# Kernel tuning notes

Hardware: AMD Instinct MI355X
Metric: run time of the kernel (lower is better)

## Reference

```python
import jax, jax.numpy as jnp
import numpy as np

N_ATOMS = 500_000
N_MOLS = 25_000
HID = 300
CONSTRAINT = 0.0  # per-molecule target total (e.g. neutral net charge)
W_SCALE = 0.05    # keep random-init activations tame


def setup_inputs() -> dict:
    key = jax.random.key(0)
    ks = jax.random.split(key, 6)
    hidden = jax.random.normal(ks[0], (N_ATOMS, HID), dtype=jnp.float32)
    seg_ids = jnp.sort(jax.random.randint(ks[1], (N_ATOMS,), 0, N_MOLS, dtype=jnp.int32))
    # output readout FFN: Linear(300->300) -> ReLU -> Linear(300->1)
    W1 = jax.random.normal(ks[2], (HID, HID), dtype=jnp.float32) * W_SCALE
    b1 = jnp.zeros((HID,), dtype=jnp.float32)
    W2 = jax.random.normal(ks[3], (HID, 1), dtype=jnp.float32) * W_SCALE
    b2 = jnp.zeros((1,), dtype=jnp.float32)
    # weights readout FFN (same architecture); bias=1 keeps segment weight sums positive
    V1 = jax.random.normal(ks[4], (HID, HID), dtype=jnp.float32) * W_SCALE
    vb1 = jnp.zeros((HID,), dtype=jnp.float32)
    V2 = jax.random.normal(ks[5], (HID, 1), dtype=jnp.float32) * W_SCALE
    vb2 = jnp.ones((1,), dtype=jnp.float32)
    return {"hidden": hidden, "seg_ids": seg_ids, "W1": W1, "b1": b1, "W2": W2,
            "b2": b2, "V1": V1, "vb1": vb1, "V2": V2, "vb2": vb2}


def _ffn(x, Wa, ba, Wb, bb):
    # dropout is identity in eval mode
    h = jax.nn.relu(x @ Wa + ba)
    return h @ Wb + bb  # [N, 1]


def reference(hidden, seg_ids, W1, b1, W2, b2, V1, vb1, V2, vb2):
    output = _ffn(hidden, W1, b1, W2, b2)    # [N, 1] raw per-atom predictions
    weights = _ffn(hidden, V1, vb1, V2, vb2) # [N, 1] per-atom correction weights
    # per-molecule segment sums (replaces the Python loop over a_scope)
    sum_o = jax.ops.segment_sum(output[:, 0], seg_ids, num_segments=N_MOLS)   # [M]
    sum_w = jax.ops.segment_sum(weights[:, 0], seg_ids, num_segments=N_MOLS)  # [M]
    sum_w = jnp.where(sum_w == 0, 1.0, sum_w)  # empty segments are skipped in the original
    corr = (CONSTRAINT - sum_o) / sum_w        # [M]
    out = output + weights * corr[seg_ids][:, None]  # [N, 1]
    return out
```

## Files before the change

### kernel.cpp

```cpp
#include <hip/hip_runtime.h>
#include <stdint.h>

#define N_ATOMS 500000
#define N_MOLS  25000
#define HID     300
#define BA      128
#define WS_ELE  102400

#define AROWB   616
#define A_BYTES (BA * AROWB)
#define B_OFF   A_BYTES
#define BUF_B   40960

typedef __attribute__((ext_vector_type(8)))  short          short8v;
typedef __attribute__((ext_vector_type(16))) float          f32x16;

static __device__ __forceinline__ unsigned short f2bf(float f) {
  unsigned int u = __float_as_uint(f);
  u += 0x7fffu + ((u >> 16) & 1u);
  return (unsigned short)(u >> 16);
}

static __device__ __forceinline__ void stage16(const char* gsrc, char* ldst, int ln) {
  __builtin_amdgcn_global_load_lds(
      (const __attribute__((address_space(1))) void*)(gsrc + ln * 16),
      (__attribute__((address_space(3))) void*)ldst, 16, 0, 0);
}

__global__ void prep_kernel(
    const float* __restrict__ W1, const float* __restrict__ V1,
    const float* __restrict__ b1, const float* __restrict__ vb1,
    const float* __restrict__ W2, const float* __restrict__ V2,
    unsigned short* __restrict__ W1s, unsigned short* __restrict__ V1s,
    float* __restrict__ b1p, float* __restrict__ vb1p,
    float* __restrict__ W2p, float* __restrict__ V2p,
    float* __restrict__ sums)
{
  const int t = blockIdx.x * 256 + threadIdx.x;
  if (t < 2 * WS_ELE) {
    const float* src = (t < WS_ELE) ? W1 : V1;
    unsigned short* dst = (t < WS_ELE) ? W1s : V1s;
    const int i    = (t < WS_ELE) ? t : t - WS_ELE;
    const int j    = i & 7;
    const int lane = (i >> 3) & 63;
    const int nt   = (i >> 9) % 10;
    const int kc16 = i / 5120;
    const int k = kc16 * 16 + (lane >> 5) * 8 + j;
    const int n = nt * 32 + (lane & 31);
    const float v = (k < HID && n < HID) ? src[k * HID + n] : 0.f;
    dst[i] = f2bf(v);
  } else if (t < 2 * WS_ELE + 1280) {
    const int i = t - 2 * WS_ELE;
    const int which = i / 320;
    const int e = i - which * 320;
    const float* s = (which == 0) ? b1 : (which == 1) ? vb1 : (which == 2) ? W2 : V2;
    float*       d = (which == 0) ? b1p : (which == 1) ? vb1p : (which == 2) ? W2p : V2p;
    d[e] = (e < HID) ? s[e] : 0.f;
  } else if (t < 2 * WS_ELE + 1280 + 2 * N_MOLS) {
    sums[t - (2 * WS_ELE + 1280)] = 0.f;
  }
}

__global__ __launch_bounds__(512, 2) void fused_ffn(
    const float* __restrict__ hidden,
    const unsigned short* __restrict__ W1s, const unsigned short* __restrict__ V1s,
    const float* __restrict__ b1p, const float* __restrict__ vb1p,
    const float* __restrict__ W2p, const float* __restrict__ V2p,
    const float* __restrict__ b2, const float* __restrict__ vb2,
    float* __restrict__ outA, float* __restrict__ outW)
{
  __shared__ char lds[A_BYTES + 2 * BUF_B];
  __shared__ float sOutA[BA];
  __shared__ float sOutW[BA];

  const int tid = (int)threadIdx.x;
  const int ln  = tid & 63;
  const int wv  = tid >> 6;
  const int mtx = wv & 1;
  const int ch  = (wv >> 1) & 1;
  const int rgh = wv >> 2;
  const int l31 = ln & 31;
  const int lh  = ln >> 5;
  const long base = (long)blockIdx.x * BA;

  {
    char* dst = lds + B_OFF;
    #pragma unroll
    for (int r = 0; r < 5; ++r) {
      const int cc = wv * 5 + r;
      const char* src = (cc < 20) ? ((const char*)W1s + cc * 1024)
                                  : ((const char*)V1s + (cc - 20) * 1024);
      stage16(src, dst + cc * 1024, ln);
    }
  }

  #pragma unroll
  for (int bt = 0; bt < 2; ++bt) {
    const int nb = bt ? 9 : 10;
    float4 tmp[10];
    #pragma unroll
    for (int m = 0; m < 10; ++m) {
      if (m >= nb) break;
      const int i   = tid + (bt * 10 + m) * 512;
      const int row = i / 76;
      const int c4  = i - row * 76;
      float4 v = make_float4(0.f, 0.f, 0.f, 0.f);
      const long atom = base + row;
      if (c4 < 75 && atom < N_ATOMS)
        v = *reinterpret_cast<const float4*>(hidden + atom * (long)HID + c4 * 4);
      tmp[m] = v;
    }
    #pragma unroll
    for (int m = 0; m < 10; ++m) {
      if (m >= nb) break;
      const int i   = tid + (bt * 10 + m) * 512;
      const int row = i / 76;
      const int c4  = i - row * 76;
      ushort4 b;
      b.x = f2bf(tmp[m].x); b.y = f2bf(tmp[m].y);
      b.z = f2bf(tmp[m].z); b.w = f2bf(tmp[m].w);
      *reinterpret_cast<ushort4*>(lds + row * AROWB + c4 * 8) = b;
    }
  }
  __syncthreads();

  f32x16 acc[2][5] = {};

  for (int c = 0; c < 10; ++c) {
    const char* buf = lds + B_OFF + (c & 1) * BUF_B;

    if (c < 9) {
      char* nbuf = lds + B_OFF + ((c + 1) & 1) * BUF_B;
      const char* wsrc = (const char*)W1s + (c + 1) * 20480;
      const char* vsrc = (const char*)V1s + (c + 1) * 20480;
      #pragma unroll
      for (int r = 0; r < 5; ++r) {
        const int cc = wv * 5 + r;
        const char* src = (cc < 20) ? (wsrc + cc * 1024) : (vsrc + (cc - 20) * 1024);
        stage16(src, nbuf + cc * 1024, ln);
      }
    }

#define DO_HALF(hh)                                                            \
    {                                                                          \
      const int kc16 = 2 * c + (hh);                                           \
      const short8v a0 = *reinterpret_cast<const short8v*>(                    \
          lds + (rgh * 64 + l31) * AROWB + kc16 * 32 + lh * 16);               \
      const short8v a1 = *reinterpret_cast<const short8v*>(                    \
          lds + (rgh * 64 + 32 + l31) * AROWB + kc16 * 32 + lh * 16);          \
      const char* bb = buf + mtx * 20480 + (hh) * 10240 + ch * 5120;           \
      _Pragma("unroll")                                                        \
      for (int nt = 0; nt < 5; ++nt) {                                         \
        const short8v bf = *reinterpret_cast<const short8v*>(                  \
            bb + nt * 1024 + ln * 16);                                         \
        acc[0][nt] = __builtin_amdgcn_mfma_f32_32x32x16_bf16(a0, bf, acc[0][nt], 0, 0, 0); \
        acc[1][nt] = __builtin_amdgcn_mfma_f32_32x32x16_bf16(a1, bf, acc[1][nt], 0, 0, 0); \
      }                                                                        \
    }
    DO_HALF(0);
    if (c < 9) DO_HALF(1);
#undef DO_HALF

    __syncthreads();
  }

  float bv[5], w2[5];
  const float* bbv = mtx ? vb1p : b1p;
  const float* ww2 = mtx ? V2p  : W2p;
  #pragma unroll
  for (int nt = 0; nt < 5; ++nt) {
    const int cix = ch * 160 + nt * 32 + l31;
    bv[nt] = bbv[cix];
    w2[nt] = ww2[cix];
  }
  if (tid < BA) { sOutA[tid] = 0.f; sOutW[tid] = 0.f; }
  __syncthreads();

  float* sOut = mtx ? sOutW : sOutA;
  #pragma unroll
  for (int rg = 0; rg < 2; ++rg) {
    #pragma unroll
    for (int r = 0; r < 16; ++r) {
      float s = 0.f;
      #pragma unroll
      for (int nt = 0; nt < 5; ++nt) {
        float x = fmaxf(acc[rg][nt][r] + bv[nt], 0.f);
        s = fmaf(x, w2[nt], s);
      }
      s += __shfl_xor(s, 1);
      s += __shfl_xor(s, 2);
      s += __shfl_xor(s, 4);
      s += __shfl_xor(s, 8);
      s += __shfl_xor(s, 16);
      if (l31 == 0) {
        const int row = rgh * 64 + rg * 32 + (r & 3) + 8 * (r >> 2) + 4 * lh;
        atomicAdd(&sOut[row], s);
      }
    }
  }
  __syncthreads();
  if (tid < BA) {
    const long atom = base + tid;
    if (atom < N_ATOMS) {
      outA[atom] = sOutA[tid] + b2[0];
      outW[atom] = sOutW[tid] + vb2[0];
    }
  }
}

__global__ void segsum_kernel(
    const float* __restrict__ outA, const float* __restrict__ outW,
    const int* __restrict__ seg,
    float* __restrict__ sum_o, float* __restrict__ sum_w)
{
  const long i0 = ((long)blockIdx.x * 256 + threadIdx.x) * 8;
  if (i0 >= N_ATOMS) return;
  const int4   s0 = *reinterpret_cast<const int4*>(seg + i0);
  const int4   s1 = *reinterpret_cast<const int4*>(seg + i0 + 4);
  const float4 o0 = *reinterpret_cast<const float4*>(outA + i0);
  const float4 o1 = *reinterpret_cast<const float4*>(outA + i0 + 4);
  const float4 w0 = *reinterpret_cast<const float4*>(outW + i0);
  const float4 w1 = *reinterpret_cast<const float4*>(outW + i0 + 4);
  const int   ss[8] = {s0.x, s0.y, s0.z, s0.w, s1.x, s1.y, s1.z, s1.w};
  const float oo[8] = {o0.x, o0.y, o0.z, o0.w, o1.x, o1.y, o1.z, o1.w};
  const float ww[8] = {w0.x, w0.y, w0.z, w0.w, w1.x, w1.y, w1.z, w1.w};
  int cur = ss[0];
  float ao = 0.f, aw = 0.f;
  #pragma unroll
  for (int j = 0; j < 8; ++j) {
    if (ss[j] != cur) {
      atomicAdd(&sum_o[cur], ao);
      atomicAdd(&sum_w[cur], aw);
      cur = ss[j]; ao = 0.f; aw = 0.f;
    }
    ao += oo[j]; aw += ww[j];
  }
  atomicAdd(&sum_o[cur], ao);
  atomicAdd(&sum_w[cur], aw);
}

__global__ void final_kernel(
    const float* __restrict__ outA, const float* __restrict__ outW,
    const int* __restrict__ seg,
    const float* __restrict__ sum_o, const float* __restrict__ sum_w,
    float* __restrict__ out)
{
  const long i0 = ((long)blockIdx.x * 256 + threadIdx.x) * 4;
  if (i0 >= N_ATOMS) return;
  const int4   s4 = *reinterpret_cast<const int4*>(seg + i0);
  const float4 o4 = *reinterpret_cast<const float4*>(outA + i0);
  const float4 w4 = *reinterpret_cast<const float4*>(outW + i0);
  const int   ss[4] = {s4.x, s4.y, s4.z, s4.w};
  const float oo[4] = {o4.x, o4.y, o4.z, o4.w};
  const float ww[4] = {w4.x, w4.y, w4.z, w4.w};
  float r[4];
  #pragma unroll
  for (int j = 0; j < 4; ++j) {
    const int s = ss[j];
    float sw = sum_w[s];
    sw = (sw == 0.f) ? 1.f : sw;
    const float corr = (0.f - sum_o[s]) / sw;
    r[j] = oo[j] + ww[j] * corr;
  }
  *reinterpret_cast<float4*>(out + i0) = make_float4(r[0], r[1], r[2], r[3]);
}

extern "C" void kernel_launch(void* const* d_in, const int* in_sizes, int n_in,
                              void* d_out, int out_size, void* d_ws, size_t ws_size,
                              hipStream_t stream)
{
  const float* hidden = (const float*)d_in[0];
  const int*   seg    = (const int*)d_in[1];
  const float* W1     = (const float*)d_in[2];
  const float* b1     = (const float*)d_in[3];
  const float* W2     = (const float*)d_in[4];
  const float* b2     = (const float*)d_in[5];
  const float* V1     = (const float*)d_in[6];
  const float* vb1    = (const float*)d_in[7];
  const float* V2     = (const float*)d_in[8];
  const float* vb2    = (const float*)d_in[9];

  char* ws = (char*)d_ws;
  float*          outA  = (float*)(ws + 0);
  float*          outW  = (float*)(ws + 2000000);
  float*          sum_o = (float*)(ws + 4000000);
  float*          sum_w = (float*)(ws + 4100000);
  unsigned short* W1s   = (unsigned short*)(ws + 4200000);
  unsigned short* V1s   = (unsigned short*)(ws + 4404800);
  float*          b1p   = (float*)(ws + 4609600);
  float*          vb1p  = (float*)(ws + 4610880);
  float*          W2p   = (float*)(ws + 4612160);
  float*          V2p   = (float*)(ws + 4613440);

  prep_kernel<<<1001, 256, 0, stream>>>(W1, V1, b1, vb1, W2, V2,
                                        W1s, V1s, b1p, vb1p, W2p, V2p, sum_o);

  const int nblk = (N_ATOMS + BA - 1) / BA;
  fused_ffn<<<nblk, 512, 0, stream>>>(hidden, W1s, V1s, b1p, vb1p, W2p, V2p,
                                      b2, vb2, outA, outW);

  segsum_kernel<<<(N_ATOMS / 8 + 255) / 256, 256, 0, stream>>>(outA, outW, seg,
                                                               sum_o, sum_w);

  final_kernel<<<(N_ATOMS / 4 + 255) / 256, 256, 0, stream>>>(outA, outW, seg,
                                                              sum_o, sum_w,
                                                              (float*)d_out);
}
```

Measured before the change: 418.6 us.

## Load weight fragments straight into registers and halve the atom tile

The fused FFN kernel no longer stages W1/V1 tiles through double-buffered LDS with global_load_lds and per-chunk barriers. Each wave now loads its B fragments directly from global (L2) into registers, prefetching the next k-chunk one step ahead. The block shrinks to 64 atoms and 256 threads, which cuts LDS use and removes the per-chunk __syncthreads. The cost is that weight traffic from L2 per atom doubles, and register pressure rises from holding the prefetched fragments. The input conversion also switches to the HIP bfloat16 intrinsic.

```diff
diff --git a/kernel.cpp b/kernel.cpp
--- a/kernel.cpp
+++ b/kernel.cpp
@@ -1,16 +1,14 @@
 #include <hip/hip_runtime.h>
+#include <hip/hip_bf16.h>
 #include <stdint.h>
 
 #define N_ATOMS 500000
 #define N_MOLS  25000
 #define HID     300
-#define BA      128
+#define BA      64
 #define WS_ELE  102400
-
+#define NCH     19
 #define AROWB   616
-#define A_BYTES (BA * AROWB)
-#define B_OFF   A_BYTES
-#define BUF_B   40960
 
 typedef __attribute__((ext_vector_type(8)))  short          short8v;
 typedef __attribute__((ext_vector_type(16))) float          f32x16;
@@ -19,12 +17,6 @@
   unsigned int u = __float_as_uint(f);
   u += 0x7fffu + ((u >> 16) & 1u);
   return (unsigned short)(u >> 16);
-}
-
-static __device__ __forceinline__ void stage16(const char* gsrc, char* ldst, int ln) {
-  __builtin_amdgcn_global_load_lds(
-      (const __attribute__((address_space(1))) void*)(gsrc + ln * 16),
-      (__attribute__((address_space(3))) void*)ldst, 16, 0, 0);
 }
 
 __global__ void prep_kernel(
@@ -61,7 +53,7 @@
   }
 }
 
-__global__ __launch_bounds__(512, 2) void fused_ffn(
+__global__ __launch_bounds__(256, 2) void fused_ffn(
     const float* __restrict__ hidden,
     const unsigned short* __restrict__ W1s, const unsigned short* __restrict__ V1s,
     const float* __restrict__ b1p, const float* __restrict__ vb1p,
@@ -69,7 +61,7 @@
     const float* __restrict__ b2, const float* __restrict__ vb2,
     float* __restrict__ outA, float* __restrict__ outW)
 {
-  __shared__ char lds[A_BYTES + 2 * BUF_B];
+  __shared__ char ldsA[BA * AROWB];
   __shared__ float sOutA[BA];
   __shared__ float sOutW[BA];
 
@@ -77,23 +69,11 @@
   const int ln  = tid & 63;
   const int wv  = tid >> 6;
   const int mtx = wv & 1;
-  const int ch  = (wv >> 1) & 1;
-  const int rgh = wv >> 2;
+  const int ch  = wv >> 1;
   const int l31 = ln & 31;
   const int lh  = ln >> 5;
   const long base = (long)blockIdx.x * BA;
 
-  {
-    char* dst = lds + B_OFF;
-    #pragma unroll
-    for (int r = 0; r < 5; ++r) {
-      const int cc = wv * 5 + r;
-      const char* src = (cc < 20) ? ((const char*)W1s + cc * 1024)
-                                  : ((const char*)V1s + (cc - 20) * 1024);
-      stage16(src, dst + cc * 1024, ln);
-    }
-  }
-
   #pragma unroll
   for (int bt = 0; bt < 2; ++bt) {
     const int nb = bt ? 9 : 10;
@@ -101,7 +81,7 @@
     #pragma unroll
     for (int m = 0; m < 10; ++m) {
       if (m >= nb) break;
-      const int i   = tid + (bt * 10 + m) * 512;
+      const int i   = tid + (bt * 10 + m) * 256;
       const int row = i / 76;
       const int c4  = i - row * 76;
       float4 v = make_float4(0.f, 0.f, 0.f, 0.f);
@@ -113,55 +93,47 @@
     #pragma unroll
     for (int m = 0; m < 10; ++m) {
       if (m >= nb) break;
-      const int i   = tid + (bt * 10 + m) * 512;
+      const int i   = tid + (bt * 10 + m) * 256;
       const int row = i / 76;
       const int c4  = i - row * 76;
       ushort4 b;
-      b.x = f2bf(tmp[m].x); b.y = f2bf(tmp[m].y);
-      b.z = f2bf(tmp[m].z); b.w = f2bf(tmp[m].w);
-      *reinterpret_cast<ushort4*>(lds + row * AROWB + c4 * 8) = b;
+      b.x = (unsigned short)__bfloat16_as_ushort(__float2bfloat16(tmp[m].x));
+      b.y = (unsigned short)__bfloat16_as_ushort(__float2bfloat16(tmp[m].y));
+      b.z = (unsigned short)__bfloat16_as_ushort(__float2bfloat16(tmp[m].z));
+      b.w = (unsigned short)__bfloat16_as_ushort(__float2bfloat16(tmp[m].w));
+      *reinterpret_cast<ushort4*>(ldsA + row * AROWB + c4 * 8) = b;
     }
   }
   __syncthreads();
 
+  const char* bwave = (mtx ? (const char*)V1s : (const char*)W1s) + ch * 5120;
+  const char* aB0 = ldsA + l31 * AROWB + lh * 16;
+  const char* aB1 = aB0 + 32 * AROWB;
+
   f32x16 acc[2][5] = {};
-
-  for (int c = 0; c < 10; ++c) {
-    const char* buf = lds + B_OFF + (c & 1) * BUF_B;
-
-    if (c < 9) {
-      char* nbuf = lds + B_OFF + ((c + 1) & 1) * BUF_B;
-      const char* wsrc = (const char*)W1s + (c + 1) * 20480;
-      const char* vsrc = (const char*)V1s + (c + 1) * 20480;
+  short8v bc[5], bn[5];
+  #pragma unroll
+  for (int nt = 0; nt < 5; ++nt)
+    bc[nt] = *reinterpret_cast<const short8v*>(bwave + nt * 1024 + ln * 16);
+
+  for (int c = 0; c < NCH; ++c) {
+    if (c < NCH - 1) {
+      const char* bsrc = bwave + (c + 1) * 10240;
       #pragma unroll
-      for (int r = 0; r < 5; ++r) {
-        const int cc = wv * 5 + r;
-        const char* src = (cc < 20) ? (wsrc + cc * 1024) : (vsrc + (cc - 20) * 1024);
-        stage16(src, nbuf + cc * 1024, ln);
-      }
-    }
-
-#define DO_HALF(hh)                                                            \
-    {                                                                          \
-      const int kc16 = 2 * c + (hh);                                           \
-      const short8v a0 = *reinterpret_cast<const short8v*>(                    \
-          lds + (rgh * 64 + l31) * AROWB + kc16 * 32 + lh * 16);               \
-      const short8v a1 = *reinterpret_cast<const short8v*>(                    \
-          lds + (rgh * 64 + 32 + l31) * AROWB + kc16 * 32 + lh * 16);          \
-      const char* bb = buf + mtx * 20480 + (hh) * 10240 + ch * 5120;           \
-      _Pragma("unroll")                                                        \
-      for (int nt = 0; nt < 5; ++nt) {                                         \
-        const short8v bf = *reinterpret_cast<const short8v*>(                  \
-            bb + nt * 1024 + ln * 16);                                         \
-        acc[0][nt] = __builtin_amdgcn_mfma_f32_32x32x16_bf16(a0, bf, acc[0][nt], 0, 0, 0); \
-        acc[1][nt] = __builtin_amdgcn_mfma_f32_32x32x16_bf16(a1, bf, acc[1][nt], 0, 0, 0); \
-      }                                                                        \
-    }
-    DO_HALF(0);
-    if (c < 9) DO_HALF(1);
-#undef DO_HALF
-
-    __syncthreads();
+      for (int nt = 0; nt < 5; ++nt)
+        bn[nt] = *reinterpret_cast<const short8v*>(bsrc + nt * 1024 + ln * 16);
+    }
+    const short8v a0 = *reinterpret_cast<const short8v*>(aB0 + c * 32);
+    const short8v a1 = *reinterpret_cast<const short8v*>(aB1 + c * 32);
+    #pragma unroll
+    for (int nt = 0; nt < 5; ++nt) {
+      acc[0][nt] = __builtin_amdgcn_mfma_f32_32x32x16_bf16(a0, bc[nt], acc[0][nt], 0, 0, 0);
+      acc[1][nt] = __builtin_amdgcn_mfma_f32_32x32x16_bf16(a1, bc[nt], acc[1][nt], 0, 0, 0);
+    }
+    if (c < NCH - 1) {
+      #pragma unroll
+      for (int nt = 0; nt < 5; ++nt) bc[nt] = bn[nt];
+    }
   }
 
   float bv[5], w2[5];
@@ -193,7 +165,7 @@
       s += __shfl_xor(s, 8);
       s += __shfl_xor(s, 16);
       if (l31 == 0) {
-        const int row = rgh * 64 + rg * 32 + (r & 3) + 8 * (r >> 2) + 4 * lh;
+        const int row = rg * 32 + (r & 3) + 8 * (r >> 2) + 4 * lh;
         atomicAdd(&sOut[row], s);
       }
     }
@@ -296,7 +268,7 @@
                                         W1s, V1s, b1p, vb1p, W2p, V2p, sum_o);
 
   const int nblk = (N_ATOMS + BA - 1) / BA;
-  fused_ffn<<<nblk, 512, 0, stream>>>(hidden, W1s, V1s, b1p, vb1p, W2p, V2p,
+  fused_ffn<<<nblk, 256, 0, stream>>>(hidden, W1s, V1s, b1p, vb1p, W2p, V2p,
                                       b2, vb2, outA, outW);
 
   segsum_kernel<<<(N_ATOMS / 8 + 255) / 256, 256, 0, stream>>>(outA, outW, seg,
```

Result: slower. 513.1 us (+22.6%).

## Double FFN block to 1024 threads, one 32-row tile per wave

Applied to the files above, without the earlier changes.

The fused FFN kernel now launches 16 waves per block instead of 8, and each wave computes a single 32-row M tile (5 accumulators) instead of two. Weight-slab staging is redistributed over 16 waves, the hidden-row load loop is reshaped for 1024 threads, and bf16 conversion uses the library intrinsic. The goal is more waves and fewer accumulator registers per wave to hide latency. In exchange each B fragment read from LDS now feeds only one MFMA instead of two, and the 1024-thread blocks lose the old two-blocks-per-CU launch bound.

```diff
diff --git a/kernel.cpp b/kernel.cpp
--- a/kernel.cpp
+++ b/kernel.cpp
@@ -1,10 +1,12 @@
 #include <hip/hip_runtime.h>
+#include <hip/hip_bf16.h>
 #include <stdint.h>
 
 #define N_ATOMS 500000
 #define N_MOLS  25000
 #define HID     300
 #define BA      128
+#define NTHR    1024
 #define WS_ELE  102400
 
 #define AROWB   616
@@ -61,7 +63,7 @@
   }
 }
 
-__global__ __launch_bounds__(512, 2) void fused_ffn(
+__global__ __launch_bounds__(NTHR) void fused_ffn(
     const float* __restrict__ hidden,
     const unsigned short* __restrict__ W1s, const unsigned short* __restrict__ V1s,
     const float* __restrict__ b1p, const float* __restrict__ vb1p,
@@ -78,91 +80,93 @@
   const int wv  = tid >> 6;
   const int mtx = wv & 1;
   const int ch  = (wv >> 1) & 1;
-  const int rgh = wv >> 2;
+  const int rg  = wv >> 2;
   const int l31 = ln & 31;
   const int lh  = ln >> 5;
   const long base = (long)blockIdx.x * BA;
 
+  const int p0 = (wv < 8) ? wv * 3 : 24 + (wv - 8) * 2;
+  const int np = (wv < 8) ? 3 : 2;
+
+#define STAGE_SLAB(cc, dstbuf) do {                                            \
+    _Pragma("unroll")                                                          \
+    for (int r_ = 0; r_ < 3; ++r_) {                                           \
+      if (r_ < np) {                                                           \
+        const int p_   = p0 + r_;                                              \
+        const int mp_  = p_ / 20;                                              \
+        const int q_   = p_ - mp_ * 20;                                        \
+        const int kk_  = q_ / 10;                                              \
+        const int nt_  = q_ - kk_ * 10;                                        \
+        const char* src_ = (mp_ ? (const char*)V1s : (const char*)W1s)         \
+                         + ((cc) * 2 + kk_) * 10240 + nt_ * 1024;              \
+        stage16(src_, (dstbuf) + p_ * 1024, ln);                               \
+      }                                                                        \
+    }                                                                          \
+  } while (0)
+
+  STAGE_SLAB(0, lds + B_OFF);
+
   {
-    char* dst = lds + B_OFF;
-    #pragma unroll
-    for (int r = 0; r < 5; ++r) {
-      const int cc = wv * 5 + r;
-      const char* src = (cc < 20) ? ((const char*)W1s + cc * 1024)
-                                  : ((const char*)V1s + (cc - 20) * 1024);
-      stage16(src, dst + cc * 1024, ln);
-    }
-  }
-
-  #pragma unroll
-  for (int bt = 0; bt < 2; ++bt) {
-    const int nb = bt ? 9 : 10;
     float4 tmp[10];
     #pragma unroll
-    for (int m = 0; m < 10; ++m) {
-      if (m >= nb) break;
-      const int i   = tid + (bt * 10 + m) * 512;
-      const int row = i / 76;
-      const int c4  = i - row * 76;
+    for (int j = 0; j < 10; ++j) {
+      const int i = tid + j * NTHR;
       float4 v = make_float4(0.f, 0.f, 0.f, 0.f);
-      const long atom = base + row;
-      if (c4 < 75 && atom < N_ATOMS)
-        v = *reinterpret_cast<const float4*>(hidden + atom * (long)HID + c4 * 4);
-      tmp[m] = v;
+      if (i < BA * 76) {
+        const int row = i / 76;
+        const int c4  = i - row * 76;
+        const long atom = base + row;
+        if (c4 < 75 && atom < N_ATOMS)
+          v = *reinterpret_cast<const float4*>(hidden + atom * (long)HID + c4 * 4);
+      }
+      tmp[j] = v;
     }
     #pragma unroll
-    for (int m = 0; m < 10; ++m) {
-      if (m >= nb) break;
-      const int i   = tid + (bt * 10 + m) * 512;
-      const int row = i / 76;
-      const int c4  = i - row * 76;
-      ushort4 b;
-      b.x = f2bf(tmp[m].x); b.y = f2bf(tmp[m].y);
-      b.z = f2bf(tmp[m].z); b.w = f2bf(tmp[m].w);
-      *reinterpret_cast<ushort4*>(lds + row * AROWB + c4 * 8) = b;
+    for (int j = 0; j < 10; ++j) {
+      const int i = tid + j * NTHR;
+      if (i < BA * 76) {
+        const int row = i / 76;
+        const int c4  = i - row * 76;
+        ushort4 b;
+        b.x = (unsigned short)__bfloat16_as_ushort(__float2bfloat16(tmp[j].x));
+        b.y = (unsigned short)__bfloat16_as_ushort(__float2bfloat16(tmp[j].y));
+        b.z = (unsigned short)__bfloat16_as_ushort(__float2bfloat16(tmp[j].z));
+        b.w = (unsigned short)__bfloat16_as_ushort(__float2bfloat16(tmp[j].w));
+        *reinterpret_cast<ushort4*>(lds + row * AROWB + c4 * 8) = b;
+      }
     }
   }
   __syncthreads();
 
-  f32x16 acc[2][5] = {};
-
-  for (int c = 0; c < 10; ++c) {
-    const char* buf = lds + B_OFF + (c & 1) * BUF_B;
-
-    if (c < 9) {
-      char* nbuf = lds + B_OFF + ((c + 1) & 1) * BUF_B;
-      const char* wsrc = (const char*)W1s + (c + 1) * 20480;
-      const char* vsrc = (const char*)V1s + (c + 1) * 20480;
-      #pragma unroll
-      for (int r = 0; r < 5; ++r) {
-        const int cc = wv * 5 + r;
-        const char* src = (cc < 20) ? (wsrc + cc * 1024) : (vsrc + (cc - 20) * 1024);
-        stage16(src, nbuf + cc * 1024, ln);
-      }
-    }
-
-#define DO_HALF(hh)                                                            \
-    {                                                                          \
-      const int kc16 = 2 * c + (hh);                                           \
-      const short8v a0 = *reinterpret_cast<const short8v*>(                    \
-          lds + (rgh * 64 + l31) * AROWB + kc16 * 32 + lh * 16);               \
-      const short8v a1 = *reinterpret_cast<const short8v*>(                    \
-          lds + (rgh * 64 + 32 + l31) * AROWB + kc16 * 32 + lh * 16);          \
-      const char* bb = buf + mtx * 20480 + (hh) * 10240 + ch * 5120;           \
-      _Pragma("unroll")                                                        \
-      for (int nt = 0; nt < 5; ++nt) {                                         \
-        const short8v bf = *reinterpret_cast<const short8v*>(                  \
-            bb + nt * 1024 + ln * 16);                                         \
-        acc[0][nt] = __builtin_amdgcn_mfma_f32_32x32x16_bf16(a0, bf, acc[0][nt], 0, 0, 0); \
-        acc[1][nt] = __builtin_amdgcn_mfma_f32_32x32x16_bf16(a1, bf, acc[1][nt], 0, 0, 0); \
-      }                                                                        \
-    }
-    DO_HALF(0);
-    if (c < 9) DO_HALF(1);
-#undef DO_HALF
-
+  f32x16 acc[5] = {};
+  const char* aBase = lds + (rg * 32 + l31) * AROWB + lh * 16;
+
+#define DO_KS(slab, kc16) do {                                                 \
+    const short8v a_ = *reinterpret_cast<const short8v*>(aBase + (kc16) * 32); \
+    const char* bb_ = (slab) + mtx * 20480 + ((kc16) & 1) * 10240 + ch * 5120; \
+    _Pragma("unroll")                                                          \
+    for (int nt_ = 0; nt_ < 5; ++nt_) {                                        \
+      const short8v bf_ = *reinterpret_cast<const short8v*>(                   \
+          bb_ + nt_ * 1024 + ln * 16);                                         \
+      acc[nt_] = __builtin_amdgcn_mfma_f32_32x32x16_bf16(a_, bf_, acc[nt_], 0, 0, 0); \
+    }                                                                          \
+  } while (0)
+
+  #pragma unroll 1
+  for (int c = 0; c < 9; ++c) {
+    const char* slab = lds + B_OFF + (c & 1) * BUF_B;
+    char*       nbuf = lds + B_OFF + ((c + 1) & 1) * BUF_B;
+    STAGE_SLAB(c + 1, nbuf);
+    DO_KS(slab, 2 * c);
+    DO_KS(slab, 2 * c + 1);
     __syncthreads();
   }
+  {
+    const char* slab = lds + B_OFF + (9 & 1) * BUF_B;
+    DO_KS(slab, 18);
+  }
+#undef DO_KS
+#undef STAGE_SLAB
 
   float bv[5], w2[5];
   const float* bbv = mtx ? vb1p : b1p;
@@ -178,24 +182,21 @@
 
   float* sOut = mtx ? sOutW : sOutA;
   #pragma unroll
-  for (int rg = 0; rg < 2; ++rg) {
+  for (int r = 0; r < 16; ++r) {
+    float s = 0.f;
     #pragma unroll
-    for (int r = 0; r < 16; ++r) {
-      float s = 0.f;
-      #pragma unroll
-      for (int nt = 0; nt < 5; ++nt) {
-        float x = fmaxf(acc[rg][nt][r] + bv[nt], 0.f);
-        s = fmaf(x, w2[nt], s);
-      }
-      s += __shfl_xor(s, 1);
-      s += __shfl_xor(s, 2);
-      s += __shfl_xor(s, 4);
-      s += __shfl_xor(s, 8);
-      s += __shfl_xor(s, 16);
-      if (l31 == 0) {
-        const int row = rgh * 64 + rg * 32 + (r & 3) + 8 * (r >> 2) + 4 * lh;
-        atomicAdd(&sOut[row], s);
-      }
+    for (int nt = 0; nt < 5; ++nt) {
+      float x = fmaxf(acc[nt][r] + bv[nt], 0.f);
+      s = fmaf(x, w2[nt], s);
+    }
+    s += __shfl_xor(s, 1);
+    s += __shfl_xor(s, 2);
+    s += __shfl_xor(s, 4);
+    s += __shfl_xor(s, 8);
+    s += __shfl_xor(s, 16);
+    if (l31 == 0) {
+      const int row = rg * 32 + (r & 3) + 8 * (r >> 2) + 4 * lh;
+      atomicAdd(&sOut[row], s);
     }
   }
   __syncthreads();
@@ -296,8 +297,8 @@
                                         W1s, V1s, b1p, vb1p, W2p, V2p, sum_o);
 
   const int nblk = (N_ATOMS + BA - 1) / BA;
-  fused_ffn<<<nblk, 512, 0, stream>>>(hidden, W1s, V1s, b1p, vb1p, W2p, V2p,
-                                      b2, vb2, outA, outW);
+  fused_ffn<<<nblk, NTHR, 0, stream>>>(hidden, W1s, V1s, b1p, vb1p, W2p, V2p,
+                                       b2, vb2, outA, outW);
 
   segsum_kernel<<<(N_ATOMS / 8 + 255) / 256, 256, 0, stream>>>(outA, outW, seg,
                                                                sum_o, sum_w);
```

After: 485.9 us. 16.1% more time.
